# Optimization experiments

Hardware: AMD Instinct MI355X
Metric: run time of the kernel (lower is better)

## Reference

```python
import jax, jax.numpy as jnp
import numpy as np
from jax import lax

B, IMG, P, STRIDE, CIN = 4, 256, 8, 8, 1
D, NH, L = 768, 8, 21
GRID = (IMG - P) // STRIDE + 1  # 32
N = GRID * GRID                 # 1024 tokens
HD = D // NH                    # 96
SCALE = float(HD) ** -0.5


def setup_inputs() -> dict:
    key = jax.random.key(0)
    ks = jax.random.split(key, 9)
    s = 0.02
    return {
        "sam": jax.random.normal(ks[0], (B, CIN, IMG, IMG), dtype=jnp.float32),
        "conv_w": jax.random.normal(ks[1], (D, CIN, P, P), dtype=jnp.float32) * s,
        "conv_b": jnp.zeros((D,), dtype=jnp.float32),
        "ln_g": jnp.ones((D,), dtype=jnp.float32),
        "ln_b": jnp.zeros((D,), dtype=jnp.float32),
        "pos": jax.random.normal(ks[2], (N, D), dtype=jnp.float32) * s,
        "q_w": jax.random.normal(ks[3], (L, D, D), dtype=jnp.float32) * s,
        "kv_w": jax.random.normal(ks[4], (L, D, 2 * D), dtype=jnp.float32) * s,
        "proj_w": jax.random.normal(ks[5], (L, D, D), dtype=jnp.float32) * s,
        "proj_b": jnp.zeros((L, D), dtype=jnp.float32),
    }


def _layernorm(x, g, b, eps=1e-5):
    mu = jnp.mean(x, axis=-1, keepdims=True)
    var = jnp.mean(jnp.square(x - mu), axis=-1, keepdims=True)
    return (x - mu) * lax.rsqrt(var + eps) * g + b


def _guidance(x, qw, kvw, pw, pb):
    b, n, c = x.shape
    q = jnp.einsum('bnc,cd->bnd', x, qw).reshape(b, n, NH, HD).transpose(0, 2, 1, 3)
    kv = jnp.einsum('bnc,cd->bnd', x, kvw)
    k = kv[..., :c].reshape(b, n, NH, HD).transpose(0, 2, 1, 3)
    v = kv[..., c:].reshape(b, n, NH, HD).transpose(0, 2, 1, 3)
    attn = jax.nn.softmax(jnp.einsum('bhnd,bhmd->bhnm', q, k) * SCALE, axis=-1)
    o = jnp.einsum('bhnm,bhmd->bhnd', attn, v).transpose(0, 2, 1, 3).reshape(b, n, c)
    o = jnp.einsum('bnc,cd->bnd', o, pw) + pb
    return o + x  # residual (dropouts are identity in eval)


def reference(sam, conv_w, conv_b, ln_g, ln_b, pos, q_w, kv_w, proj_w, proj_b):
    # Patch embed: conv (valid, stride=patch) -> [B,D,32,32] -> tokens -> LN
    y = lax.conv_general_dilated(sam, conv_w, window_strides=(STRIDE, STRIDE),
                                 padding='VALID',
                                 dimension_numbers=('NCHW', 'OIHW', 'NCHW'))
    y = y + conv_b[None, :, None, None]
    y = y.reshape(B, D, N).transpose(0, 2, 1)  # [B,N,D]
    y = _layernorm(y, ln_g, ln_b)
    x0 = y + pos[None]  # pos_embed(arange) broadcast over batch
    # Faithful to source: each block consumes the SAME x0; output is last block's.
    out = x0
    for i in range(L):
        out = _guidance(x0, q_w[i], kv_w[i], proj_w[i], proj_b[i])
    return out
```

## Files before the change

kernel.cpp:

```cpp
#include <hip/hip_runtime.h>
#include <hip/hip_bf16.h>

typedef __attribute__((ext_vector_type(4))) float f32x4;
typedef __attribute__((ext_vector_type(8))) short s16x8;
typedef unsigned short u16;
typedef unsigned int u32;

#define DEV __device__ __forceinline__

DEV u16 f2bf(float f) {
  union { float f; u32 u; } v; v.f = f;
  u32 r = v.u + 0x7fffu + ((v.u >> 16) & 1u);
  return (u16)(r >> 16);
}

#define MFMA16(a, b, c) __builtin_amdgcn_mfma_f32_16x16x32_bf16((a), (b), (c), 0, 0, 0)
#define GLD16(g, l) __builtin_amdgcn_global_load_lds((const __attribute__((address_space(1))) u32*)(g), (__attribute__((address_space(3))) u32*)(l), 16, 0, 0)

#define QSCALE 0.10206207261596577f

__global__ __launch_bounds__(256) void prep_k(
    const float* __restrict__ qw, const float* __restrict__ kvw,
    const float* __restrict__ pw, u16* __restrict__ wqkvT, u16* __restrict__ pwT,
    const float* __restrict__ sam, const float* __restrict__ cw,
    const float* __restrict__ cb, const float* __restrict__ g,
    const float* __restrict__ bb, const float* __restrict__ pos,
    float* __restrict__ x0f, u16* __restrict__ x0b) {
  __shared__ float tb[32][33];
  __shared__ float pix[4][64];
  __shared__ float red[2][4][4];
  int bid = blockIdx.x;
  if (bid < 2304) {
    int ct = bid / 24, kt = (bid % 24) * 32;
    const float* src;
    u16* dst;
    int ncols, tn, dstbase;
    float scale = 1.0f;
    if (ct < 24) {
      src = qw; ncols = 768; tn = ct * 32; dst = wqkvT; dstbase = tn; scale = QSCALE;
    } else if (ct < 72) {
      src = kvw; ncols = 1536; tn = (ct - 24) * 32; dst = wqkvT; dstbase = 768 + tn;
    } else {
      src = pw; ncols = 768; tn = (ct - 72) * 32; dst = pwT; dstbase = tn;
    }
    int tx = threadIdx.x & 31, ty = threadIdx.x >> 5;
#pragma unroll
    for (int i = 0; i < 4; i++)
      tb[ty + i * 8][tx] = src[(size_t)(kt + ty + i * 8) * ncols + tn + tx];
    __syncthreads();
#pragma unroll
    for (int i = 0; i < 4; i++)
      dst[(size_t)(dstbase + ty + i * 8) * 768 + kt + tx] = f2bf(tb[tx][ty + i * 8] * scale);
    return;
  }
  int blk = bid - 2304;
  int b = blk >> 8, nq = blk & 255;
  int t = threadIdx.x;
  {
    int tk = t >> 6, p = t & 63;
    int n = nq * 4 + tk;
    int gi = n >> 5, gj = n & 31;
    pix[tk][p] = sam[b * 65536 + (gi * 8 + (p >> 3)) * 256 + gj * 8 + (p & 7)];
  }
  __syncthreads();
  float acc[3][4];
#pragma unroll
  for (int u = 0; u < 3; u++) {
    int d = t + u * 256;
    const float4* w4 = (const float4*)(cw + (size_t)d * 64);
    float a0 = cb[d];
    float av0 = a0, av1 = a0, av2 = a0, av3 = a0;
#pragma unroll
    for (int pc = 0; pc < 16; pc++) {
      float4 w = w4[pc];
      av0 += w.x * pix[0][pc * 4] + w.y * pix[0][pc * 4 + 1] + w.z * pix[0][pc * 4 + 2] + w.w * pix[0][pc * 4 + 3];
      av1 += w.x * pix[1][pc * 4] + w.y * pix[1][pc * 4 + 1] + w.z * pix[1][pc * 4 + 2] + w.w * pix[1][pc * 4 + 3];
      av2 += w.x * pix[2][pc * 4] + w.y * pix[2][pc * 4 + 1] + w.z * pix[2][pc * 4 + 2] + w.w * pix[2][pc * 4 + 3];
      av3 += w.x * pix[3][pc * 4] + w.y * pix[3][pc * 4 + 1] + w.z * pix[3][pc * 4 + 2] + w.w * pix[3][pc * 4 + 3];
    }
    acc[u][0] = av0; acc[u][1] = av1; acc[u][2] = av2; acc[u][3] = av3;
  }
  float s1[4], s2[4];
#pragma unroll
  for (int tk = 0; tk < 4; tk++) {
    s1[tk] = acc[0][tk] + acc[1][tk] + acc[2][tk];
    s2[tk] = acc[0][tk] * acc[0][tk] + acc[1][tk] * acc[1][tk] + acc[2][tk] * acc[2][tk];
  }
#pragma unroll
  for (int m = 1; m < 64; m <<= 1) {
#pragma unroll
    for (int tk = 0; tk < 4; tk++) {
      s1[tk] += __shfl_xor(s1[tk], m);
      s2[tk] += __shfl_xor(s2[tk], m);
    }
  }
  int wid = t >> 6;
  if ((t & 63) == 0) {
#pragma unroll
    for (int tk = 0; tk < 4; tk++) { red[0][wid][tk] = s1[tk]; red[1][wid][tk] = s2[tk]; }
  }
  __syncthreads();
  float mu[4], rs[4];
#pragma unroll
  for (int tk = 0; tk < 4; tk++) {
    float S1 = red[0][0][tk] + red[0][1][tk] + red[0][2][tk] + red[0][3][tk];
    float S2 = red[1][0][tk] + red[1][1][tk] + red[1][2][tk] + red[1][3][tk];
    mu[tk] = S1 * (1.0f / 768.0f);
    float var = S2 * (1.0f / 768.0f) - mu[tk] * mu[tk];
    rs[tk] = rsqrtf(var + 1e-5f);
  }
#pragma unroll
  for (int u = 0; u < 3; u++) {
    int d = t + u * 256;
    float gg = g[d], bbv = bb[d];
#pragma unroll
    for (int tk = 0; tk < 4; tk++) {
      int n = nq * 4 + tk;
      float val = (acc[u][tk] - mu[tk]) * rs[tk] * gg + bbv + pos[(size_t)n * 768 + d];
      size_t idx = ((size_t)(b * 1024 + n)) * 768 + d;
      x0f[idx] = val;
      x0b[idx] = f2bf(val);
    }
  }
}

template <int EPI>
__global__ __launch_bounds__(256, 2) void gemm128(
    const u16* __restrict__ A, const u16* __restrict__ BT, int M, int N, int K,
    u16* __restrict__ q, u16* __restrict__ kk_, u16* __restrict__ vt,
    const float* __restrict__ pb, const float* __restrict__ x0f,
    float* __restrict__ outp) {
  __shared__ __align__(16) u16 Al[2][128 * 32];
  __shared__ __align__(16) u16 Bl[2][128 * 32];
  int m0 = blockIdx.y * 128, n0 = blockIdx.x * 128;
  int tid = threadIdx.x, lane = tid & 63, wid = tid >> 6;
  int wr = wid >> 1, wc = wid & 1;
  f32x4 acc[4][4] = {};
  int arow = lane >> 2, acol = (lane & 3) * 8;
  const u16* ag = A + (size_t)(m0 + wid * 32 + arow) * K + acol;
  const u16* bg = BT + (size_t)(n0 + wid * 32 + arow) * K + acol;
  int lofs = wid * 32 * 32;
#define STAGE_G(bufi, kk)                              \
  do {                                                 \
    GLD16(ag + (kk), &Al[bufi][lofs]);                 \
    GLD16(ag + (kk) + 16 * K, &Al[bufi][lofs + 512]);  \
    GLD16(bg + (kk), &Bl[bufi][lofs]);                 \
    GLD16(bg + (kk) + 16 * K, &Bl[bufi][lofs + 512]);  \
  } while (0)
  STAGE_G(0, 0);
  int nk = K >> 5;
  int cur = 0;
  for (int t = 0; t < nk; t++) {
    __syncthreads();
    if (t + 1 < nk) STAGE_G(cur ^ 1, (t + 1) * 32);
    s16x8 af[4], bf[4];
#pragma unroll
    for (int m = 0; m < 4; m++)
      af[m] = *(const s16x8*)&Al[cur][(wr * 64 + m * 16 + (lane & 15)) * 32 + (lane >> 4) * 8];
#pragma unroll
    for (int nn = 0; nn < 4; nn++)
      bf[nn] = *(const s16x8*)&Bl[cur][(wc * 64 + nn * 16 + (lane & 15)) * 32 + (lane >> 4) * 8];
#pragma unroll
    for (int m = 0; m < 4; m++)
#pragma unroll
      for (int nn = 0; nn < 4; nn++)
        acc[m][nn] = MFMA16(af[m], bf[nn], acc[m][nn]);
    cur ^= 1;
  }
#undef STAGE_G
#pragma unroll
  for (int m = 0; m < 4; m++) {
    int rbase = m0 + wr * 64 + m * 16 + ((lane >> 4) << 2);
#pragma unroll
    for (int nn = 0; nn < 4; nn++) {
      int col = n0 + wc * 64 + nn * 16 + (lane & 15);
      f32x4 v = acc[m][nn];
      if (EPI == 0) {
        if (col < 1536) {
          int cc = (col < 768) ? col : col - 768;
          int h = cc / 96, hd = cc % 96;
          u16* dst = (col < 768) ? q : kk_;
          int bq = (rbase >> 10) * 8 + h;
#pragma unroll
          for (int i = 0; i < 4; i++) {
            int row = rbase + i;
            dst[((size_t)bq * 1024 + (row & 1023)) * 96 + hd] = f2bf(v[i]);
          }
        } else {
          int cc = col - 1536;
          int h = cc / 96, hd = cc % 96;
          int bq = (rbase >> 10) * 8 + h;
          ushort4 pk;
          pk.x = f2bf(v[0]); pk.y = f2bf(v[1]); pk.z = f2bf(v[2]); pk.w = f2bf(v[3]);
          *(ushort4*)&vt[((size_t)bq * 96 + hd) * 1024 + (rbase & 1023)] = pk;
        }
      } else {
        float add = pb[col];
#pragma unroll
        for (int i = 0; i < 4; i++) {
          size_t idx = (size_t)(rbase + i) * 768 + col;
          outp[idx] = v[i] + add + x0f[idx];
        }
      }
    }
  }
}

__global__ __launch_bounds__(256, 2) void attn_k(
    const u16* __restrict__ qg, const u16* __restrict__ kg,
    const u16* __restrict__ vg, u16* __restrict__ o) {
  int newid = ((blockIdx.x & 7) << 6) + (blockIdx.x >> 3);
  int bh = newid >> 4, qb = newid & 15;
  int b = bh >> 3, h = bh & 7;
  int tid = threadIdx.x, lane = tid & 63, wid = tid >> 6;
  int l15 = lane & 15, l4 = lane >> 4;
  int q0 = qb * 64 + wid * 16;
  const u16* qbase = qg + (size_t)bh * 1024 * 96;
  const u16* kbase = kg + (size_t)bh * 1024 * 96;
  const u16* vbase = vg + (size_t)bh * 96 * 1024;
  s16x8 aq[3];
#pragma unroll
  for (int kc = 0; kc < 3; kc++)
    aq[kc] = *(const s16x8*)&qbase[(size_t)(q0 + l15) * 96 + kc * 32 + l4 * 8];
  float mrun[4], lrun[4];
  f32x4 accO[6] = {};
#pragma unroll
  for (int i = 0; i < 4; i++) { mrun[i] = -1e30f; lrun[i] = 0.0f; }
  __shared__ __align__(16) u16 Kl[64][104];
  __shared__ __align__(16) u16 Pl[4][16][72];
  int kkey[3], koff[3];
#pragma unroll
  for (int it = 0; it < 3; it++) {
    int c = it * 256 + tid;
    kkey[it] = c / 12; koff[it] = (c % 12) * 8;
  }
  for (int kt = 0; kt < 16; kt++) {
#pragma unroll
    for (int it = 0; it < 3; it++)
      *(uint4*)&Kl[kkey[it]][koff[it]] =
          *(const uint4*)&kbase[(size_t)(kt * 64 + kkey[it]) * 96 + koff[it]];
    __syncthreads();
    s16x8 bv[6][2];
#pragma unroll
    for (int nf = 0; nf < 6; nf++)
#pragma unroll
      for (int kc = 0; kc < 2; kc++)
        bv[nf][kc] = *(const s16x8*)&vbase[(size_t)(nf * 16 + l15) * 1024 +
                                           kt * 64 + kc * 32 + l4 * 8];
    f32x4 s4[4] = {};
    __builtin_amdgcn_s_setprio(1);
#pragma unroll
    for (int nf = 0; nf < 4; nf++)
#pragma unroll
      for (int kc = 0; kc < 3; kc++) {
        s16x8 bk = *(const s16x8*)&Kl[nf * 16 + l15][kc * 32 + l4 * 8];
        s4[nf] = MFMA16(aq[kc], bk, s4[nf]);
      }
    __builtin_amdgcn_s_setprio(0);
    float rm[4];
#pragma unroll
    for (int i = 0; i < 4; i++) {
      rm[i] = fmaxf(fmaxf(s4[0][i], s4[1][i]), fmaxf(s4[2][i], s4[3][i]));
#pragma unroll
      for (int m = 1; m < 16; m <<= 1) rm[i] = fmaxf(rm[i], __shfl_xor(rm[i], m));
    }
    bool need = (rm[0] > mrun[0]) || (rm[1] > mrun[1]) ||
                (rm[2] > mrun[2]) || (rm[3] > mrun[3]);
    if (__any(need)) {
#pragma unroll
      for (int i = 0; i < 4; i++) {
        float newm = fmaxf(mrun[i], rm[i]);
        float al = __expf(mrun[i] - newm);
        mrun[i] = newm;
        lrun[i] *= al;
#pragma unroll
        for (int nf = 0; nf < 6; nf++) accO[nf][i] *= al;
      }
    }
#pragma unroll
    for (int i = 0; i < 4; i++) {
      float ps = 0.0f;
#pragma unroll
      for (int nf = 0; nf < 4; nf++) {
        float p = __expf(s4[nf][i] - mrun[i]);
        s4[nf][i] = p;
        ps += p;
      }
#pragma unroll
      for (int m = 1; m < 16; m <<= 1) ps += __shfl_xor(ps, m);
      lrun[i] += ps;
    }
#pragma unroll
    for (int nf = 0; nf < 4; nf++)
#pragma unroll
      for (int i = 0; i < 4; i++)
        Pl[wid][l4 * 4 + i][nf * 16 + l15] = f2bf(s4[nf][i]);
    asm volatile("s_waitcnt lgkmcnt(0)" ::: "memory");
    __builtin_amdgcn_sched_barrier(0);
    __builtin_amdgcn_s_setprio(1);
#pragma unroll
    for (int kc = 0; kc < 2; kc++) {
      s16x8 ap = *(const s16x8*)&Pl[wid][l15][kc * 32 + l4 * 8];
#pragma unroll
      for (int nf = 0; nf < 6; nf++)
        accO[nf] = MFMA16(ap, bv[nf][kc], accO[nf]);
    }
    __builtin_amdgcn_s_setprio(0);
    __syncthreads();
  }
#pragma unroll
  for (int i = 0; i < 4; i++) {
    float inv = 1.0f / lrun[i];
    int tok = q0 + l4 * 4 + i;
    u16* orow = o + ((size_t)(b * 1024 + tok)) * 768 + h * 96;
#pragma unroll
    for (int nf = 0; nf < 6; nf++)
      orow[nf * 16 + l15] = f2bf(accO[nf][i] * inv);
  }
}

extern "C" void kernel_launch(void* const* d_in, const int* in_sizes, int n_in,
                              void* d_out, int out_size, void* d_ws, size_t ws_size,
                              hipStream_t stream) {
  const float* sam    = (const float*)d_in[0];
  const float* conv_w = (const float*)d_in[1];
  const float* conv_b = (const float*)d_in[2];
  const float* ln_g   = (const float*)d_in[3];
  const float* ln_b   = (const float*)d_in[4];
  const float* pos    = (const float*)d_in[5];
  const float* q_w    = (const float*)d_in[6] + (size_t)20 * 768 * 768;
  const float* kv_w   = (const float*)d_in[7] + (size_t)20 * 768 * 1536;
  const float* proj_w = (const float*)d_in[8] + (size_t)20 * 768 * 768;
  const float* proj_b = (const float*)d_in[9] + (size_t)20 * 768;

  char* ws = (char*)d_ws;
  float* x0f  = (float*)ws; ws += (size_t)4096 * 768 * 4;
  u16* x0b    = (u16*)ws;   ws += (size_t)4096 * 768 * 2;
  u16* wqkvT  = (u16*)ws;   ws += (size_t)2304 * 768 * 2;
  u16* pwT    = (u16*)ws;   ws += (size_t)768 * 768 * 2;
  u16* qs     = (u16*)ws;   ws += (size_t)32 * 1024 * 96 * 2;
  u16* ks     = (u16*)ws;   ws += (size_t)32 * 1024 * 96 * 2;
  u16* vts    = (u16*)ws;   ws += (size_t)32 * 96 * 1024 * 2;
  u16* ob     = (u16*)ws;   ws += (size_t)4096 * 768 * 2;

  prep_k<<<3328, 256, 0, stream>>>(q_w, kv_w, proj_w, wqkvT, pwT, sam, conv_w,
                                   conv_b, ln_g, ln_b, pos, x0f, x0b);
  dim3 g1(18, 32);
  gemm128<0><<<g1, 256, 0, stream>>>(x0b, wqkvT, 4096, 2304, 768, qs, ks, vts,
                                     nullptr, nullptr, nullptr);
  attn_k<<<512, 256, 0, stream>>>(qs, ks, vts, ob);
  dim3 g2(6, 32);
  gemm128<1><<<g2, 256, 0, stream>>>(ob, pwT, 4096, 768, 768, nullptr, nullptr,
                                     nullptr, proj_b, x0f, (float*)d_out);
}
```

Baseline: 337.5 us.

## Move patch-embed conv to MFMA kernel and drop fp32 residual buffer

Splits the preparation kernel in two. The first converts the weights plus the conv weights and image patches to bf16 in a swizzled layout. A new conv+LayerNorm kernel runs the patch-embedding conv as bf16 MFMA over 16-token tiles, replacing the scalar fp32 FMA loop. The fp32 x0 copy is removed and the projection epilogue reads the bf16 x0 for the residual, cutting memory traffic at the cost of lower precision in the conv and the residual add.

```diff
diff --git a/kernel.cpp b/kernel.cpp
--- a/kernel.cpp
+++ b/kernel.cpp
@@ -13,23 +13,24 @@
   u32 r = v.u + 0x7fffu + ((v.u >> 16) & 1u);
   return (u16)(r >> 16);
 }
+DEV float bf2f(u16 h) {
+  union { u32 u; float f; } v; v.u = ((u32)h) << 16;
+  return v.f;
+}
 
 #define MFMA16(a, b, c) __builtin_amdgcn_mfma_f32_16x16x32_bf16((a), (b), (c), 0, 0, 0)
 #define GLD16(g, l) __builtin_amdgcn_global_load_lds((const __attribute__((address_space(1))) u32*)(g), (__attribute__((address_space(3))) u32*)(l), 16, 0, 0)
 
 #define QSCALE 0.10206207261596577f
 
-__global__ __launch_bounds__(256) void prep_k(
+__global__ __launch_bounds__(256) void prep0_k(
     const float* __restrict__ qw, const float* __restrict__ kvw,
     const float* __restrict__ pw, u16* __restrict__ wqkvT, u16* __restrict__ pwT,
-    const float* __restrict__ sam, const float* __restrict__ cw,
-    const float* __restrict__ cb, const float* __restrict__ g,
-    const float* __restrict__ bb, const float* __restrict__ pos,
-    float* __restrict__ x0f, u16* __restrict__ x0b) {
+    const float* __restrict__ cw, u16* __restrict__ cwb,
+    const float* __restrict__ sam, u16* __restrict__ apx) {
   __shared__ float tb[32][33];
-  __shared__ float pix[4][64];
-  __shared__ float red[2][4][4];
   int bid = blockIdx.x;
+  int tid = threadIdx.x;
   if (bid < 2304) {
     int ct = bid / 24, kt = (bid % 24) * 32;
     const float* src;
@@ -43,7 +44,7 @@
     } else {
       src = pw; ncols = 768; tn = (ct - 72) * 32; dst = pwT; dstbase = tn;
     }
-    int tx = threadIdx.x & 31, ty = threadIdx.x >> 5;
+    int tx = tid & 31, ty = tid >> 5;
 #pragma unroll
     for (int i = 0; i < 4; i++)
       tb[ty + i * 8][tx] = src[(size_t)(kt + ty + i * 8) * ncols + tn + tx];
@@ -53,73 +54,114 @@
       dst[(size_t)(dstbase + ty + i * 8) * 768 + kt + tx] = f2bf(tb[tx][ty + i * 8] * scale);
     return;
   }
-  int blk = bid - 2304;
-  int b = blk >> 8, nq = blk & 255;
-  int t = threadIdx.x;
+  if (bid < 2316) {
+    int e0 = (bid - 2304) * 4096 + tid * 16;
+    int n = e0 >> 6, k0 = e0 & 63;
+    int sx = (n & 7) << 3;
+    u16 tmp[16];
+#pragma unroll
+    for (int j = 0; j < 16; j++) tmp[j] = f2bf(cw[e0 + j]);
+#pragma unroll
+    for (int h = 0; h < 2; h++)
+      *(uint4*)&cwb[n * 64 + ((k0 + h * 8) ^ sx)] = *(const uint4*)&tmp[h * 8];
+    return;
+  }
+  int blk = bid - 2316;
+  int b = blk >> 5, gi = blk & 31;
+  const float* srow = sam + ((size_t)b * 256 + gi * 8) * 256;
+  int gj = tid >> 3, c = tid & 7;
+#pragma unroll
+  for (int r = 0; r < 8; r++) {
+    float v = srow[r * 256 + tid];
+    apx[((size_t)b * 1024 + gi * 32 + gj) * 64 + r * 8 + c] = f2bf(v);
+  }
+}
+
+__global__ __launch_bounds__(256) void convln_k(
+    const u16* __restrict__ apx, const u16* __restrict__ cwb,
+    const float* __restrict__ cb, const float* __restrict__ g,
+    const float* __restrict__ bb, const float* __restrict__ pos,
+    u16* __restrict__ x0b) {
+  __shared__ __align__(16) u16 Bl[768 * 64];
+  __shared__ __align__(16) u16 Al[16 * 72];
+  __shared__ float red[4][16][2];
+  int tid = threadIdx.x, lane = tid & 63, wid = tid >> 6;
+  int l15 = lane & 15, l4 = lane >> 4;
+  int tok0 = blockIdx.x * 16;
   {
-    int tk = t >> 6, p = t & 63;
-    int n = nq * 4 + tk;
-    int gi = n >> 5, gj = n & 31;
-    pix[tk][p] = sam[b * 65536 + (gi * 8 + (p >> 3)) * 256 + gj * 8 + (p & 7)];
+    const u16* gsrc = cwb + wid * 512 + lane * 8;
+    u16* ldst = Bl + wid * 512;
+#pragma unroll
+    for (int it = 0; it < 24; it++)
+      GLD16(gsrc + it * 2048, ldst + it * 2048);
+  }
+  if (tid < 128) {
+    int row = tid >> 3, ch = (tid & 7) * 8;
+    *(uint4*)&Al[row * 72 + ch] = *(const uint4*)&apx[(size_t)(tok0 + row) * 64 + ch];
   }
   __syncthreads();
-  float acc[3][4];
-#pragma unroll
-  for (int u = 0; u < 3; u++) {
-    int d = t + u * 256;
-    const float4* w4 = (const float4*)(cw + (size_t)d * 64);
-    float a0 = cb[d];
-    float av0 = a0, av1 = a0, av2 = a0, av3 = a0;
-#pragma unroll
-    for (int pc = 0; pc < 16; pc++) {
-      float4 w = w4[pc];
-      av0 += w.x * pix[0][pc * 4] + w.y * pix[0][pc * 4 + 1] + w.z * pix[0][pc * 4 + 2] + w.w * pix[0][pc * 4 + 3];
-      av1 += w.x * pix[1][pc * 4] + w.y * pix[1][pc * 4 + 1] + w.z * pix[1][pc * 4 + 2] + w.w * pix[1][pc * 4 + 3];
-      av2 += w.x * pix[2][pc * 4] + w.y * pix[2][pc * 4 + 1] + w.z * pix[2][pc * 4 + 2] + w.w * pix[2][pc * 4 + 3];
-      av3 += w.x * pix[3][pc * 4] + w.y * pix[3][pc * 4 + 1] + w.z * pix[3][pc * 4 + 2] + w.w * pix[3][pc * 4 + 3];
-    }
-    acc[u][0] = av0; acc[u][1] = av1; acc[u][2] = av2; acc[u][3] = av3;
-  }
-  float s1[4], s2[4];
-#pragma unroll
-  for (int tk = 0; tk < 4; tk++) {
-    s1[tk] = acc[0][tk] + acc[1][tk] + acc[2][tk];
-    s2[tk] = acc[0][tk] * acc[0][tk] + acc[1][tk] * acc[1][tk] + acc[2][tk] * acc[2][tk];
-  }
-#pragma unroll
-  for (int m = 1; m < 64; m <<= 1) {
-#pragma unroll
-    for (int tk = 0; tk < 4; tk++) {
-      s1[tk] += __shfl_xor(s1[tk], m);
-      s2[tk] += __shfl_xor(s2[tk], m);
-    }
-  }
-  int wid = t >> 6;
-  if ((t & 63) == 0) {
-#pragma unroll
-    for (int tk = 0; tk < 4; tk++) { red[0][wid][tk] = s1[tk]; red[1][wid][tk] = s2[tk]; }
-  }
+  s16x8 af[2];
+#pragma unroll
+  for (int kc = 0; kc < 2; kc++)
+    af[kc] = *(const s16x8*)&Al[l15 * 72 + kc * 32 + l4 * 8];
+  f32x4 s[12];
+#pragma unroll
+  for (int nt = 0; nt < 12; nt++) {
+    int row = wid * 192 + nt * 16 + l15;
+    int sx = (row & 7) << 3;
+    s16x8 b0 = *(const s16x8*)&Bl[row * 64 + ((l4 * 8) ^ sx)];
+    s16x8 b1 = *(const s16x8*)&Bl[row * 64 + ((32 + l4 * 8) ^ sx)];
+    f32x4 a = {};
+    a = MFMA16(af[0], b0, a);
+    a = MFMA16(af[1], b1, a);
+    s[nt] = a;
+  }
+  float p1[4] = {0, 0, 0, 0}, p2[4] = {0, 0, 0, 0};
+#pragma unroll
+  for (int nt = 0; nt < 12; nt++) {
+    float cbv = cb[wid * 192 + nt * 16 + l15];
+#pragma unroll
+    for (int i = 0; i < 4; i++) {
+      float y = s[nt][i] + cbv;
+      s[nt][i] = y;
+      p1[i] += y;
+      p2[i] += y * y;
+    }
+  }
+#pragma unroll
+  for (int m = 1; m < 16; m <<= 1)
+#pragma unroll
+    for (int i = 0; i < 4; i++) {
+      p1[i] += __shfl_xor(p1[i], m);
+      p2[i] += __shfl_xor(p2[i], m);
+    }
+  if (l15 == 0)
+#pragma unroll
+    for (int i = 0; i < 4; i++) {
+      red[wid][l4 * 4 + i][0] = p1[i];
+      red[wid][l4 * 4 + i][1] = p2[i];
+    }
   __syncthreads();
   float mu[4], rs[4];
 #pragma unroll
-  for (int tk = 0; tk < 4; tk++) {
-    float S1 = red[0][0][tk] + red[0][1][tk] + red[0][2][tk] + red[0][3][tk];
-    float S2 = red[1][0][tk] + red[1][1][tk] + red[1][2][tk] + red[1][3][tk];
-    mu[tk] = S1 * (1.0f / 768.0f);
-    float var = S2 * (1.0f / 768.0f) - mu[tk] * mu[tk];
-    rs[tk] = rsqrtf(var + 1e-5f);
-  }
-#pragma unroll
-  for (int u = 0; u < 3; u++) {
-    int d = t + u * 256;
-    float gg = g[d], bbv = bb[d];
-#pragma unroll
-    for (int tk = 0; tk < 4; tk++) {
-      int n = nq * 4 + tk;
-      float val = (acc[u][tk] - mu[tk]) * rs[tk] * gg + bbv + pos[(size_t)n * 768 + d];
-      size_t idx = ((size_t)(b * 1024 + n)) * 768 + d;
-      x0f[idx] = val;
-      x0b[idx] = f2bf(val);
+  for (int i = 0; i < 4; i++) {
+    int row = l4 * 4 + i;
+    float S1 = red[0][row][0] + red[1][row][0] + red[2][row][0] + red[3][row][0];
+    float S2 = red[0][row][1] + red[1][row][1] + red[2][row][1] + red[3][row][1];
+    mu[i] = S1 * (1.0f / 768.0f);
+    float var = S2 * (1.0f / 768.0f) - mu[i] * mu[i];
+    rs[i] = rsqrtf(var + 1e-5f);
+  }
+#pragma unroll
+  for (int nt = 0; nt < 12; nt++) {
+    int col = wid * 192 + nt * 16 + l15;
+    float gg = g[col], bbv = bb[col];
+#pragma unroll
+    for (int i = 0; i < 4; i++) {
+      int tok = tok0 + l4 * 4 + i;
+      float val = (s[nt][i] - mu[i]) * rs[i] * gg + bbv +
+                  pos[(size_t)(tok & 1023) * 768 + col];
+      x0b[(size_t)tok * 768 + col] = f2bf(val);
     }
   }
 }
@@ -128,7 +170,7 @@
 __global__ __launch_bounds__(256, 2) void gemm128(
     const u16* __restrict__ A, const u16* __restrict__ BT, int M, int N, int K,
     u16* __restrict__ q, u16* __restrict__ kk_, u16* __restrict__ vt,
-    const float* __restrict__ pb, const float* __restrict__ x0f,
+    const float* __restrict__ pb, const u16* __restrict__ resb,
     float* __restrict__ outp) {
   __shared__ __align__(16) u16 Al[2][128 * 32];
   __shared__ __align__(16) u16 Bl[2][128 * 32];
@@ -199,7 +241,7 @@
 #pragma unroll
         for (int i = 0; i < 4; i++) {
           size_t idx = (size_t)(rbase + i) * 768 + col;
-          outp[idx] = v[i] + add + x0f[idx];
+          outp[idx] = v[i] + add + bf2f(resb[idx]);
         }
       }
     }
@@ -334,22 +376,24 @@
   const float* proj_b = (const float*)d_in[9] + (size_t)20 * 768;
 
   char* ws = (char*)d_ws;
-  float* x0f  = (float*)ws; ws += (size_t)4096 * 768 * 4;
   u16* x0b    = (u16*)ws;   ws += (size_t)4096 * 768 * 2;
   u16* wqkvT  = (u16*)ws;   ws += (size_t)2304 * 768 * 2;
   u16* pwT    = (u16*)ws;   ws += (size_t)768 * 768 * 2;
+  u16* cwb    = (u16*)ws;   ws += (size_t)768 * 64 * 2;
+  u16* apx    = (u16*)ws;   ws += (size_t)4096 * 64 * 2;
   u16* qs     = (u16*)ws;   ws += (size_t)32 * 1024 * 96 * 2;
   u16* ks     = (u16*)ws;   ws += (size_t)32 * 1024 * 96 * 2;
   u16* vts    = (u16*)ws;   ws += (size_t)32 * 96 * 1024 * 2;
   u16* ob     = (u16*)ws;   ws += (size_t)4096 * 768 * 2;
 
-  prep_k<<<3328, 256, 0, stream>>>(q_w, kv_w, proj_w, wqkvT, pwT, sam, conv_w,
-                                   conv_b, ln_g, ln_b, pos, x0f, x0b);
+  prep0_k<<<2444, 256, 0, stream>>>(q_w, kv_w, proj_w, wqkvT, pwT,
+                                    conv_w, cwb, sam, apx);
+  convln_k<<<256, 256, 0, stream>>>(apx, cwb, conv_b, ln_g, ln_b, pos, x0b);
   dim3 g1(18, 32);
   gemm128<0><<<g1, 256, 0, stream>>>(x0b, wqkvT, 4096, 2304, 768, qs, ks, vts,
                                      nullptr, nullptr, nullptr);
   attn_k<<<512, 256, 0, stream>>>(qs, ks, vts, ob);
   dim3 g2(6, 32);
   gemm128<1><<<g2, 256, 0, stream>>>(ob, pwT, 4096, 768, 768, nullptr, nullptr,
-                                     nullptr, proj_b, x0f, (float*)d_out);
-}
+                                     nullptr, proj_b, x0b, (float*)d_out);
+}
```

Result: faster. 296.0 us (-12.3%).
